# Kernel optimization log

Hardware: AMD Instinct MI355X
Metric: run time of the kernel (lower is better)

Reference implementation:

```python
import jax, jax.numpy as jnp
import numpy as np

N_NODES = 100000
N_EDGES = 1600000
IN_FEATS = 256
OUT_FEATS = 128


def setup_inputs() -> dict:
    key = jax.random.key(0)
    k1, k2, k3, k4 = jax.random.split(key, 4)
    feat = jax.random.normal(k1, (N_NODES, IN_FEATS), dtype=jnp.float32)
    src = jax.random.randint(k2, (N_EDGES,), 0, N_NODES, dtype=jnp.int64)
    dst = jax.random.randint(k3, (N_EDGES,), 0, N_NODES, dtype=jnp.int64)
    W = jax.random.normal(k4, (IN_FEATS, OUT_FEATS), dtype=jnp.float32) * (1.0 / np.sqrt(IN_FEATS))
    b = jnp.zeros((OUT_FEATS,), dtype=jnp.float32)
    return {"feat": feat, "src": src, "dst": dst, "W": W, "b": b}


def reference(feat, src, dst, W, b):
    # norm = 'both': symmetric degree normalization, clip degrees at 1
    ones = jnp.ones((src.shape[0],), dtype=jnp.float32)
    out_deg = jax.ops.segment_sum(ones, src, num_segments=N_NODES)  # out-degree per src node
    in_deg = jax.ops.segment_sum(ones, dst, num_segments=N_NODES)   # in-degree per dst node
    norm_src = jnp.power(jnp.clip(out_deg, 1.0, None), -0.5)[:, None]  # (N,1)
    norm_dst = jnp.power(jnp.clip(in_deg, 1.0, None), -0.5)[:, None]   # (N,1)

    h = feat * norm_src
    # in_feats (256) > out_feats (128): apply W before aggregation
    h = h @ W  # (N, out_feats)
    # copy_src + sum aggregation over edges (SpMM)
    msgs = h[src]  # (E, out_feats)
    rst = jax.ops.segment_sum(msgs, dst, num_segments=N_NODES)  # (N, out_feats)
    rst = rst * norm_dst
    rst = rst + b
    return rst
```

## Files before the change

### kernel.cpp

```cpp
#include <hip/hip_runtime.h>
#include <hip/hip_bf16.h>
#include <cstddef>

#define NN 100000
#define NE 1600000
#define INF 256
#define OUTF 128
#define NBKT 196
#define BSH 9
#define P1B 250
#define EPB 6400
#define SCL (NBKT * P1B)
#define SCLP 49152

typedef __bf16 bf16x8 __attribute__((ext_vector_type(8)));
typedef float f32x4 __attribute__((ext_vector_type(4)));

__device__ __forceinline__ float bflo(uint v) { return __uint_as_float(v << 16); }
__device__ __forceinline__ float bfhi(uint v) { return __uint_as_float(v & 0xffff0000u); }

__device__ __forceinline__ void gload16(const void* g, void* l) {
  __builtin_amdgcn_global_load_lds((const __attribute__((address_space(1))) void*)g,
                                   (__attribute__((address_space(3))) void*)l, 16, 0, 0);
}

__global__ __launch_bounds__(256) void k_p1a(const int* __restrict__ src,
                                             const int* __restrict__ dst,
                                             int* __restrict__ ghd,
                                             int* __restrict__ ghs,
                                             const float* __restrict__ W,
                                             __bf16* __restrict__ Wt) {
  if (blockIdx.x >= P1B) {
    int i = (blockIdx.x - P1B) * 256 + threadIdx.x;
    if (i < SCLP - SCL) { ghd[SCL + i] = 0; ghs[SCL + i] = 0; }
    int n = i & 127, k = i >> 7;
    Wt[n * INF + k] = (__bf16)W[k * OUTF + n];
    return;
  }
  __shared__ int lhd[NBKT], lhs[NBKT];
  const int t = threadIdx.x;
  if (t < NBKT) { lhd[t] = 0; lhs[t] = 0; }
  __syncthreads();
  const int base = blockIdx.x * EPB;
#pragma unroll
  for (int i = 0; i < EPB / 256; ++i) {
    int e = base + i * 256 + t;
    atomicAdd(&lhd[dst[e] >> BSH], 1);
    atomicAdd(&lhs[src[e] >> BSH], 1);
  }
  __syncthreads();
  if (t < NBKT) {
    ghd[t * P1B + blockIdx.x] = lhd[t];
    ghs[t * P1B + blockIdx.x] = lhs[t];
  }
}

__global__ __launch_bounds__(1024) void k_p1b(int* __restrict__ ghd,
                                              int* __restrict__ ghs,
                                              int* __restrict__ row_start) {
  int* a = blockIdx.x ? ghs : ghd;
  __shared__ int wsum[16];
  const int t = threadIdx.x;
  const int lane = t & 63, wid = t >> 6;
  int4 v[12];
  const int4* p = (const int4*)(a + t * 48);
#pragma unroll
  for (int i = 0; i < 12; ++i) v[i] = p[i];
  int s = 0;
#pragma unroll
  for (int i = 0; i < 12; ++i) s += v[i].x + v[i].y + v[i].z + v[i].w;
  const int mysum = s;
#pragma unroll
  for (int d = 1; d < 64; d <<= 1) {
    int u = __shfl_up(s, d);
    if (lane >= d) s += u;
  }
  if (lane == 63) wsum[wid] = s;
  __syncthreads();
  if (wid == 0) {
    int ws = (lane < 16) ? wsum[lane] : 0;
    int inc = ws;
#pragma unroll
    for (int d = 1; d < 16; d <<= 1) {
      int u = __shfl_up(inc, d);
      if (lane >= d) inc += u;
    }
    if (lane < 16) wsum[lane] = inc - ws;
  }
  __syncthreads();
  int ex = wsum[wid] + s - mysum;
#pragma unroll
  for (int i = 0; i < 12; ++i) {
    int4 w;
    w.x = ex; ex += v[i].x;
    w.y = ex; ex += v[i].y;
    w.z = ex; ex += v[i].z;
    w.w = ex; ex += v[i].w;
    ((int4*)(a + t * 48))[i] = w;
  }
  if (blockIdx.x == 0 && t == 0) row_start[NN] = NE;
}

__global__ __launch_bounds__(256) void k_p1c(const int* __restrict__ src,
                                             const int* __restrict__ dst,
                                             const int* __restrict__ ghd,
                                             const int* __restrict__ ghs,
                                             uint* __restrict__ rec_d,
                                             ushort* __restrict__ rec_s) {
  __shared__ int od[NBKT], os[NBKT];
  const int t = threadIdx.x;
  if (t < NBKT) {
    od[t] = ghd[t * P1B + blockIdx.x];
    os[t] = ghs[t * P1B + blockIdx.x];
  }
  __syncthreads();
  const int base = blockIdx.x * EPB;
#pragma unroll
  for (int i = 0; i < EPB / 256; ++i) {
    int e = base + i * 256 + t;
    int s = src[e], d = dst[e];
    int p = atomicAdd(&od[d >> BSH], 1);
    rec_d[p] = ((uint)s << BSH) | (uint)(d & 511);
    int q = atomicAdd(&os[s >> BSH], 1);
    rec_s[q] = (ushort)(s & 511);
  }
}

__global__ __launch_bounds__(256) void k_p2(const int* __restrict__ ghd,
                                            const int* __restrict__ ghs,
                                            const uint* __restrict__ rec_d,
                                            const ushort* __restrict__ rec_s,
                                            int* __restrict__ edge_src,
                                            int* __restrict__ row_start,
                                            float* __restrict__ ns) {
  __shared__ int lh[512];
  __shared__ int sc[256];
  const int k = blockIdx.x, t = threadIdx.x;
  {
    const int base = ghd[k * P1B];
    const int end = (k == NBKT - 1) ? NE : ghd[(k + 1) * P1B];
    lh[t] = 0; lh[t + 256] = 0;
    __syncthreads();
    for (int j = base + t; j < end; j += 256) atomicAdd(&lh[rec_d[j] & 511], 1);
    __syncthreads();
    int a0 = lh[2 * t], a1 = lh[2 * t + 1];
    sc[t] = a0 + a1;
    __syncthreads();
    for (int off = 1; off < 256; off <<= 1) {
      int add = (t >= off) ? sc[t - off] : 0;
      __syncthreads();
      sc[t] += add;
      __syncthreads();
    }
    int ex = t ? sc[t - 1] : 0;
    int e0 = ex, e1 = ex + a0;
    int n0 = k * 512 + 2 * t;
    if (n0 < NN) row_start[n0] = base + e0;
    if (n0 + 1 < NN) row_start[n0 + 1] = base + e1;
    __syncthreads();
    lh[2 * t] = base + e0;
    lh[2 * t + 1] = base + e1;
    __syncthreads();
    for (int j = base + t; j < end; j += 256) {
      uint r = rec_d[j];
      int p = atomicAdd(&lh[r & 511], 1);
      edge_src[p] = (int)(r >> BSH);
    }
  }
  __syncthreads();
  {
    const int base = ghs[k * P1B];
    const int end = (k == NBKT - 1) ? NE : ghs[(k + 1) * P1B];
    lh[t] = 0; lh[t + 256] = 0;
    __syncthreads();
    for (int j = base + t; j < end; j += 256) atomicAdd(&lh[rec_s[j]], 1);
    __syncthreads();
    int n0 = k * 512 + t, n1 = n0 + 256;
    if (n0 < NN) { int c = lh[t];       ns[n0] = rsqrtf((float)(c > 1 ? c : 1)); }
    if (n1 < NN) { int c = lh[t + 256]; ns[n1] = rsqrtf((float)(c > 1 ? c : 1)); }
  }
}

__global__ __launch_bounds__(256, 4) void k_gemm(const float* __restrict__ feat,
                                                 const __bf16* __restrict__ Wt,
                                                 const float* __restrict__ ns,
                                                 __bf16* __restrict__ h) {
  __shared__ float lA[2][64 * 64];
  const int tid = threadIdx.x;
  const int w = tid >> 6, l = tid & 63;
  const int lr = l & 15, lg = l >> 4;
  const int bm = blockIdx.x * 64;

#define STAGE(b, t)                                                            \
  {                                                                            \
    _Pragma("unroll")                                                          \
    for (int i = 0; i < 4; ++i) {                                              \
      int chunk = i * 256 + tid;                                               \
      int row = chunk >> 4, cp = chunk & 15;                                   \
      int gr = bm + row; if (gr >= NN) gr = NN - 1;                            \
      int sc = cp ^ (row & 7);                                                 \
      gload16(feat + (size_t)gr * INF + (t) * 64 + sc * 4,                     \
              &lA[b][0] + (size_t)chunk * 4);                                  \
    }                                                                          \
  }

  STAGE(0, 0);

  f32x4 acc[8];
#pragma unroll
  for (int j = 0; j < 8; ++j) acc[j] = (f32x4)0.0f;

  __syncthreads();

  for (int t = 0; t < 4; ++t) {
    if (t < 3) STAGE((t + 1) & 1, t + 1);
    const float* lb = &lA[t & 1][0];
    const __bf16* bp = Wt + (size_t)lr * INF + t * 64 + lg * 8;
    bf16x8 bfrag[2][8];
#pragma unroll
    for (int kk = 0; kk < 2; ++kk)
#pragma unroll
      for (int nf = 0; nf < 8; ++nf)
        bfrag[kk][nf] = *(const bf16x8*)(bp + (size_t)nf * 16 * INF + kk * 32);
#pragma unroll
    for (int kk = 0; kk < 2; ++kk) {
      int row = w * 16 + lr;
      int c = kk * 8 + lg * 2;
      f32x4 x0 = *(const f32x4*)(lb + row * 64 + ((c ^ (row & 7)) << 2));
      f32x4 x1 = *(const f32x4*)(lb + row * 64 + (((c + 1) ^ (row & 7)) << 2));
      bf16x8 a;
#pragma unroll
      for (int j = 0; j < 4; ++j) {
        a[j] = (__bf16)x0[j];
        a[4 + j] = (__bf16)x1[j];
      }
#pragma unroll
      for (int nf = 0; nf < 8; ++nf)
        acc[nf] = __builtin_amdgcn_mfma_f32_16x16x32_bf16(a, bfrag[kk][nf], acc[nf], 0, 0, 0);
    }
    __syncthreads();
  }

#pragma unroll
  for (int r = 0; r < 4; ++r) {
    int row = bm + w * 16 + lg * 4 + r;
    if (row < NN) {
      float nsv = ns[row];
      __bf16* hp = h + (size_t)row * OUTF + lr;
#pragma unroll
      for (int nf = 0; nf < 8; ++nf)
        hp[nf * 16] = (__bf16)(acc[nf][r] * nsv);
    }
  }
#undef STAGE
}

__global__ __launch_bounds__(256) void k_aggr(const uint4* __restrict__ h4,
                                              const int* __restrict__ row_start,
                                              const int* __restrict__ edge_src,
                                              const float* __restrict__ bias,
                                              float* __restrict__ out) {
  const int wave = threadIdx.x >> 6;
  const int lane = threadIdx.x & 63;
  const int q = lane >> 4;
  const int cl = lane & 15;
  const int n = blockIdx.x * 4 + wave;
  const int s0 = row_start[n];
  const int s1 = row_start[n + 1];
  const int cnt = s1 - s0;

  float a0 = 0.f, a1 = 0.f, a2 = 0.f, a3 = 0.f, a4 = 0.f, a5 = 0.f, a6 = 0.f, a7 = 0.f;
  for (int j0 = 0; j0 < cnt; j0 += 64) {
    int nb = cnt - j0; if (nb > 64) nb = 64;
    int idv = 0;
    if (lane < nb) idv = edge_src[s0 + j0 + lane];
#pragma unroll 8
    for (int j = 0; j < nb; j += 4) {
      int jj = j + q;
      int e = __shfl(idv, jj);
      if (jj < nb) {
        uint4 v = h4[(size_t)e * 16 + cl];
        a0 += bflo(v.x); a1 += bfhi(v.x);
        a2 += bflo(v.y); a3 += bfhi(v.y);
        a4 += bflo(v.z); a5 += bfhi(v.z);
        a6 += bflo(v.w); a7 += bfhi(v.w);
      }
    }
  }
  a0 += __shfl_xor(a0, 16); a1 += __shfl_xor(a1, 16); a2 += __shfl_xor(a2, 16); a3 += __shfl_xor(a3, 16);
  a4 += __shfl_xor(a4, 16); a5 += __shfl_xor(a5, 16); a6 += __shfl_xor(a6, 16); a7 += __shfl_xor(a7, 16);
  a0 += __shfl_xor(a0, 32); a1 += __shfl_xor(a1, 32); a2 += __shfl_xor(a2, 32); a3 += __shfl_xor(a3, 32);
  a4 += __shfl_xor(a4, 32); a5 += __shfl_xor(a5, 32); a6 += __shfl_xor(a6, 32); a7 += __shfl_xor(a7, 32);

  if (q == 0) {
    float ndv = rsqrtf((float)(cnt > 1 ? cnt : 1));
    const float4* b4 = (const float4*)bias;
    float4 ba = b4[2 * cl], bb = b4[2 * cl + 1];
    float4 o0, o1;
    o0.x = a0 * ndv + ba.x; o0.y = a1 * ndv + ba.y; o0.z = a2 * ndv + ba.z; o0.w = a3 * ndv + ba.w;
    o1.x = a4 * ndv + bb.x; o1.y = a5 * ndv + bb.y; o1.z = a6 * ndv + bb.z; o1.w = a7 * ndv + bb.w;
    float4* op = (float4*)(out + (size_t)n * OUTF);
    op[2 * cl] = o0;
    op[2 * cl + 1] = o1;
  }
}

extern "C" void kernel_launch(void* const* d_in, const int* in_sizes, int n_in,
                              void* d_out, int out_size, void* d_ws, size_t ws_size,
                              hipStream_t stream) {
  const float* feat = (const float*)d_in[0];
  const int* src = (const int*)d_in[1];
  const int* dst = (const int*)d_in[2];
  const float* Wm = (const float*)d_in[3];
  const float* bias = (const float*)d_in[4];
  float* out = (float*)d_out;

  char* ws = (char*)d_ws;
  __bf16* h        = (__bf16*)(ws + 0);
  __bf16* Wt       = (__bf16*)(ws + 25600000);
  int*    ghd      = (int*)(ws + 25665536);
  int*    ghs      = (int*)(ws + 25862144);
  uint*   rec_d    = (uint*)(ws + 26058752);
  ushort* rec_s    = (ushort*)(ws + 32458752);
  int*    edge_src = (int*)(ws + 35658752);
  int*    row_start= (int*)(ws + 42058752);
  float*  ns       = (float*)(ws + 42458768);

  k_p1a<<<P1B + 128, 256, 0, stream>>>(src, dst, ghd, ghs, Wm, Wt);
  k_p1b<<<2, 1024, 0, stream>>>(ghd, ghs, row_start);
  k_p1c<<<P1B, 256, 0, stream>>>(src, dst, ghd, ghs, rec_d, rec_s);
  k_p2<<<NBKT, 256, 0, stream>>>(ghd, ghs, rec_d, rec_s, edge_src, row_start, ns);
  k_gemm<<<(NN + 63) / 64, 256, 0, stream>>>(feat, Wt, ns, h);
  k_aggr<<<NN / 4, 256, 0, stream>>>((const uint4*)h, row_start, edge_src, bias, out);
}
```

Before: 202.0 us.

## Stage full W in LDS and stream A directly from global in GEMM

The GEMM kernel now loads the whole bf16 weight matrix (64KB) into swizzled shared memory once per block. Each wave reads its feature rows straight from global memory into registers, with a one-step register prefetch, instead of staging feature tiles through LDS with global_load_lds double buffering. Blocks grow to 512 threads and 128 rows, so each W copy serves more rows. The 64KB LDS per block limits blocks per CU, and the uncoalesced per-lane row loads of A may raise global load cost.

Measured after the change: 167.9 us. 1.2x faster.

```diff
diff --git a/kernel.cpp b/kernel.cpp
--- a/kernel.cpp
+++ b/kernel.cpp
@@ -18,11 +18,6 @@
 
 __device__ __forceinline__ float bflo(uint v) { return __uint_as_float(v << 16); }
 __device__ __forceinline__ float bfhi(uint v) { return __uint_as_float(v & 0xffff0000u); }
-
-__device__ __forceinline__ void gload16(const void* g, void* l) {
-  __builtin_amdgcn_global_load_lds((const __attribute__((address_space(1))) void*)g,
-                                   (__attribute__((address_space(3))) void*)l, 16, 0, 0);
-}
 
 __global__ __launch_bounds__(256) void k_p1a(const int* __restrict__ src,
                                              const int* __restrict__ dst,
@@ -181,69 +176,60 @@
   }
 }
 
-__global__ __launch_bounds__(256, 4) void k_gemm(const float* __restrict__ feat,
+__global__ __launch_bounds__(512, 4) void k_gemm(const float* __restrict__ feat,
                                                  const __bf16* __restrict__ Wt,
                                                  const float* __restrict__ ns,
                                                  __bf16* __restrict__ h) {
-  __shared__ float lA[2][64 * 64];
+  __shared__ __attribute__((aligned(16))) char lB[65536];
   const int tid = threadIdx.x;
   const int w = tid >> 6, l = tid & 63;
-  const int lr = l & 15, lg = l >> 4;
-  const int bm = blockIdx.x * 64;
-
-#define STAGE(b, t)                                                            \
-  {                                                                            \
-    _Pragma("unroll")                                                          \
-    for (int i = 0; i < 4; ++i) {                                              \
-      int chunk = i * 256 + tid;                                               \
-      int row = chunk >> 4, cp = chunk & 15;                                   \
-      int gr = bm + row; if (gr >= NN) gr = NN - 1;                            \
-      int sc = cp ^ (row & 7);                                                 \
-      gload16(feat + (size_t)gr * INF + (t) * 64 + sc * 4,                     \
-              &lA[b][0] + (size_t)chunk * 4);                                  \
-    }                                                                          \
-  }
-
-  STAGE(0, 0);
+  const int lr = l & 15, kg = l >> 4;
+  const int row0 = blockIdx.x * 128 + w * 16;
+
+#pragma unroll
+  for (int i = 0; i < 8; ++i) {
+    int c = i * 512 + tid;
+    int col = c >> 5, g = c & 31;
+    bf16x8 v = *(const bf16x8*)(Wt + (size_t)col * INF + g * 8);
+    *(bf16x8*)(lB + col * 512 + ((g ^ (col & 7)) * 16)) = v;
+  }
+  __syncthreads();
+
+  int r0 = row0 + lr; if (r0 >= NN) r0 = NN - 1;
+  const float4* ap4k = (const float4*)(feat + (size_t)r0 * INF) + kg * 2;
 
   f32x4 acc[8];
 #pragma unroll
   for (int j = 0; j < 8; ++j) acc[j] = (f32x4)0.0f;
 
-  __syncthreads();
-
-  for (int t = 0; t < 4; ++t) {
-    if (t < 3) STAGE((t + 1) & 1, t + 1);
-    const float* lb = &lA[t & 1][0];
-    const __bf16* bp = Wt + (size_t)lr * INF + t * 64 + lg * 8;
-    bf16x8 bfrag[2][8];
-#pragma unroll
-    for (int kk = 0; kk < 2; ++kk)
-#pragma unroll
-      for (int nf = 0; nf < 8; ++nf)
-        bfrag[kk][nf] = *(const bf16x8*)(bp + (size_t)nf * 16 * INF + kk * 32);
-#pragma unroll
-    for (int kk = 0; kk < 2; ++kk) {
-      int row = w * 16 + lr;
-      int c = kk * 8 + lg * 2;
-      f32x4 x0 = *(const f32x4*)(lb + row * 64 + ((c ^ (row & 7)) << 2));
-      f32x4 x1 = *(const f32x4*)(lb + row * 64 + (((c + 1) ^ (row & 7)) << 2));
-      bf16x8 a;
-#pragma unroll
-      for (int j = 0; j < 4; ++j) {
-        a[j] = (__bf16)x0[j];
-        a[4 + j] = (__bf16)x1[j];
-      }
-#pragma unroll
-      for (int nf = 0; nf < 8; ++nf)
-        acc[nf] = __builtin_amdgcn_mfma_f32_16x16x32_bf16(a, bfrag[kk][nf], acc[nf], 0, 0, 0);
-    }
-    __syncthreads();
+  const char* bb = lB + lr * 512;
+  const int lx = lr & 7;
+
+  float4 c0 = ap4k[0], c1 = ap4k[1];
+#pragma unroll
+  for (int kk = 0; kk < 8; ++kk) {
+    float4 n0, n1;
+    if (kk < 7) {
+      n0 = ap4k[(kk + 1) * 8];
+      n1 = ap4k[(kk + 1) * 8 + 1];
+    }
+    bf16x8 a;
+#pragma unroll
+    for (int j = 0; j < 4; ++j) {
+      a[j] = (__bf16)c0[j];
+      a[4 + j] = (__bf16)c1[j];
+    }
+#pragma unroll
+    for (int nf = 0; nf < 8; ++nf) {
+      bf16x8 b = *(const bf16x8*)(bb + nf * 8192 + (((kk * 4 + kg) ^ lx) * 16));
+      acc[nf] = __builtin_amdgcn_mfma_f32_16x16x32_bf16(a, b, acc[nf], 0, 0, 0);
+    }
+    c0 = n0; c1 = n1;
   }
 
 #pragma unroll
   for (int r = 0; r < 4; ++r) {
-    int row = bm + w * 16 + lg * 4 + r;
+    int row = row0 + kg * 4 + r;
     if (row < NN) {
       float nsv = ns[row];
       __bf16* hp = h + (size_t)row * OUTF + lr;
@@ -252,7 +238,6 @@
         hp[nf * 16] = (__bf16)(acc[nf][r] * nsv);
     }
   }
-#undef STAGE
 }
 
 __global__ __launch_bounds__(256) void k_aggr(const uint4* __restrict__ h4,
@@ -330,6 +315,6 @@
   k_p1b<<<2, 1024, 0, stream>>>(ghd, ghs, row_start);
   k_p1c<<<P1B, 256, 0, stream>>>(src, dst, ghd, ghs, rec_d, rec_s);
   k_p2<<<NBKT, 256, 0, stream>>>(ghd, ghs, rec_d, rec_s, edge_src, row_start, ns);
-  k_gemm<<<(NN + 63) / 64, 256, 0, stream>>>(feat, Wt, ns, h);
+  k_gemm<<<(NN + 127) / 128, 512, 0, stream>>>(feat, Wt, ns, h);
   k_aggr<<<NN / 4, 256, 0, stream>>>((const uint4*)h, row_start, edge_src, bias, out);
 }
```
